# Kernel tuning notes

Measured on AMD Instinct MI355X. Metric: run time of the kernel, lower is better.

Reference implementation:

```python
import jax, jax.numpy as jnp
import numpy as np
import math

HGT, WID = 24, 24          # shape2d
NUM_HEADS = 12
EMB = 768
HEAD_DIM = EMB // NUM_HEADS
N_GRID = HGT * WID         # 576 spatial tokens
N_TOK = N_GRID + 1         # +1 CLS token
BATCH = 32


def _rel_indices(h: int, w: int) -> np.ndarray:
    """[(h*w), (h*w)] indices into the (2h-1)*(2w-1) relative table."""
    y = np.arange(h)
    x = np.arange(w)
    y1, x1, y2, x2 = np.meshgrid(y, x, y, x, indexing='ij')
    idx = (y1 - y2 + h - 1) * (2 * w - 1) + (x1 - x2 + w - 1)
    return idx.reshape(h * w, h * w)


def setup_inputs() -> dict:
    key = jax.random.key(0)
    ks = jax.random.split(key, 6)
    s = 0.02
    return {
        "x": jax.random.normal(ks[0], (BATCH, N_TOK, EMB), dtype=jnp.float32),
        "Wq": jax.random.normal(ks[1], (EMB, EMB), dtype=jnp.float32) * s,
        "bq": jnp.zeros((EMB,), dtype=jnp.float32),
        "Wk": jax.random.normal(ks[2], (EMB, EMB), dtype=jnp.float32) * s,
        "bk": jnp.zeros((EMB,), dtype=jnp.float32),
        "Wv": jax.random.normal(ks[3], (EMB, EMB), dtype=jnp.float32) * s,
        "bv": jnp.zeros((EMB,), dtype=jnp.float32),
        "Wp": jax.random.normal(ks[4], (EMB, EMB), dtype=jnp.float32) * s,
        "bp": jnp.zeros((EMB,), dtype=jnp.float32),
        "rel_table": jax.random.normal(ks[5], ((2 * HGT - 1) * (2 * WID - 1), NUM_HEADS), dtype=jnp.float32) * s,
    }


def reference(x, Wq, bq, Wk, bk, Wv, bv, Wp, bp, rel_table):
    B, N, E = x.shape
    scale = 1.0 / math.sqrt(HEAD_DIM)

    def heads(t):  # [B,N,E] -> [B,H,N,hd]
        return t.reshape(B, N, NUM_HEADS, HEAD_DIM).transpose(0, 2, 1, 3)

    q = heads(x @ Wq.T + bq)
    k = heads(x @ Wk.T + bk)
    v = heads(x @ Wv.T + bv)

    scores = jnp.einsum('bhqd,bhkd->bhqk', q, k) * scale  # [B,H,N,N]

    # relative position bias on spatial tokens (skip CLS row/col)
    idx = jnp.asarray(_rel_indices(HGT, WID))              # [Ng,Ng]
    bias = rel_table[idx].transpose(2, 0, 1)               # [H,Ng,Ng]
    scores = scores.at[:, :, 1:, 1:].add(bias)

    attn = jax.nn.softmax(scores, axis=-1)
    out = jnp.einsum('bhqk,bhkd->bhqd', attn, v)           # [B,H,N,hd]
    out = out.transpose(0, 2, 1, 3).reshape(B, N, E)
    return out @ Wp.T + bp
```

## Files before the change

### kernel.cpp

```cpp
#include <hip/hip_runtime.h>
#include <hip/hip_bf16.h>
#include <stdint.h>

#define HGT   24
#define WID   24
#define NHEAD 12
#define EMB   768
#define HD    64
#define NGRID 576
#define NTOK  577
#define NPAD  640
#define BATCH 32
#define MROWS (BATCH * NTOK)
#define NKT   10
#define NIT   5
#define NQT   5
#define QKVC  (3 * EMB)

typedef __attribute__((ext_vector_type(8))) short bf16x8;
typedef __attribute__((ext_vector_type(4))) float f32x4;

__device__ __forceinline__ short f2bf(float f) {
    union { float f; unsigned u; } c; c.f = f;
    unsigned r = (c.u + 0x7FFFu + ((c.u >> 16) & 1u)) >> 16;
    return (short)(r & 0xFFFFu);
}
__device__ __forceinline__ float b2f(short s) {
    union { unsigned u; float f; } c; c.u = ((unsigned)(unsigned short)s) << 16;
    return c.f;
}
__device__ __forceinline__ unsigned pk2bf(float a, float b) {
    __hip_bfloat162 h = __float22bfloat162_rn(make_float2(a, b));
    union { __hip_bfloat162 h; unsigned u; } c; c.h = h;
    return c.u;
}
__device__ __forceinline__ float fexp2(float x) {
#if __has_builtin(__builtin_amdgcn_exp2f)
    return __builtin_amdgcn_exp2f(x);
#else
    return __expf(x * 0.69314718f);
#endif
}

__device__ __forceinline__ void gload16(void* lds, const void* g) {
    __builtin_amdgcn_global_load_lds(
        (const __attribute__((address_space(1))) void*)g,
        (__attribute__((address_space(3))) void*)lds, 16, 0, 0);
}

__device__ __forceinline__ void wait_vm0_barrier() {
    asm volatile("s_waitcnt vmcnt(0)" ::: "memory");
    __builtin_amdgcn_s_barrier();
}

__device__ __forceinline__ int xcd_swizzle(int orig, int nwg) {
    int q = nwg >> 3, r = nwg & 7;
    int xcd = orig & 7, idx = orig >> 3;
    return (xcd < r) ? xcd * (q + 1) + idx : r * (q + 1) + (xcd - r) * q + idx;
}

__global__ void cast_f32_bf16(const float* __restrict__ src, short* __restrict__ dst, int n) {
    int i = (blockIdx.x * blockDim.x + threadIdx.x) * 4;
    int stride = gridDim.x * blockDim.x * 4;
    for (int j = i; j < n; j += stride) {
        float4 v = *(const float4*)(src + j);
        uint2 o;
        o.x = pk2bf(v.x, v.y);
        o.y = pk2bf(v.z, v.w);
        *(uint2*)(dst + j) = o;
    }
}

__global__ void bias_expand(const float* __restrict__ rel, short* __restrict__ be) {
    const float L2E = 1.44269504f;
    int q = blockIdx.x;
    int k = threadIdx.x;
    float v[NHEAD];
    if (k >= NTOK) {
#pragma unroll
        for (int h = 0; h < NHEAD; h++) v[h] = -1e30f;
    } else if (q == 0 || q >= NTOK || k == 0) {
#pragma unroll
        for (int h = 0; h < NHEAD; h++) v[h] = 0.f;
    } else {
        int i = q - 1, j = k - 1;
        int idx = ((i / WID) - (j / WID) + HGT - 1) * (2 * WID - 1)
                + ((i % WID) - (j % WID) + WID - 1);
        const float* rp = rel + (size_t)idx * NHEAD;
#pragma unroll
        for (int h = 0; h < NHEAD; h++) v[h] = rp[h];
    }
#pragma unroll
    for (int h = 0; h < NHEAD; h++)
        be[((size_t)h * NPAD + q) * NPAD + k] = f2bf(v[h] * L2E);
}

template <int MODE>
__global__ __launch_bounds__(512) void gemm_bt(
    const short* __restrict__ A, const short* __restrict__ Bw,
    const float* __restrict__ b0, const float* __restrict__ b1, const float* __restrict__ b2,
    void* __restrict__ Outp, short* __restrict__ vout, int M)
{
    constexpr int NC  = (MODE == 0) ? QKVC : EMB;
    constexpr int NBX = NC / 256;
    constexpr int K   = EMB;
    constexpr int NST = K / 32;

    __shared__ __align__(16) short Asl[4][256][32];
    __shared__ __align__(16) short Bsl[4][256][32];

    const int t    = threadIdx.x;
    const int lane = t & 63;
    const int w    = t >> 6;
    const int wm   = w >> 2;
    const int wn   = w & 3;
    const int lg   = lane >> 4;
    const int li   = lane & 15;

    const int nwg  = NBX * ((MROWS + 255) / 256);
    const int wgid = xcd_swizzle(blockIdx.x, nwg);
    const int tm   = (wgid / NBX) * 256;
    const int tn   = (wgid % NBX) * 256;

    const int drow = lane >> 2;
    const int lc   = (lane & 3) ^ ((lane >> 3) & 3);
    const int xsw  = (li >> 1) & 3;

    const short* agp[2];
    const short* bgp[2];
#pragma unroll
    for (int gi = 0; gi < 2; gi++) {
        int rm = tm + gi * 128 + w * 16 + drow; if (rm >= M) rm = M - 1;
        agp[gi] = A  + (size_t)rm * K + lc * 8;
        bgp[gi] = Bw + (size_t)(tn + gi * 128 + w * 16 + drow) * K + lc * 8;
    }

    f32x4 acc[8][4];
#pragma unroll
    for (int i = 0; i < 8; i++)
#pragma unroll
        for (int j = 0; j < 4; j++) acc[i][j] = (f32x4){0.f, 0.f, 0.f, 0.f};

#pragma unroll
    for (int ss = 0; ss < 3; ss++) {
        gload16(&Asl[ss][0 * 128 + w * 16][0], agp[0] + ss * 32);
        gload16(&Asl[ss][1 * 128 + w * 16][0], agp[1] + ss * 32);
        gload16(&Bsl[ss][0 * 128 + w * 16][0], bgp[0] + ss * 32);
        gload16(&Bsl[ss][1 * 128 + w * 16][0], bgp[1] + ss * 32);
    }

    for (int s = 0; s < NST; s++) {
        if (s < NST - 2)       asm volatile("s_waitcnt vmcnt(8)" ::: "memory");
        else if (s == NST - 2) asm volatile("s_waitcnt vmcnt(4)" ::: "memory");
        else                   asm volatile("s_waitcnt vmcnt(0)" ::: "memory");
        __builtin_amdgcn_s_barrier();

        const int cb = s & 3;
        bf16x8 af[8], bfv[4];
#pragma unroll
        for (int mi = 0; mi < 8; mi++)
            af[mi] = *(const bf16x8*)&Asl[cb][wm * 128 + mi * 16 + li][(lg ^ xsw) * 8];
#pragma unroll
        for (int nj = 0; nj < 4; nj++)
            bfv[nj] = *(const bf16x8*)&Bsl[cb][wn * 64 + nj * 16 + li][(lg ^ xsw) * 8];

        if (s + 3 < NST) {
            const int tb = (s + 3) & 3;
            const int ko = (s + 3) * 32;
            gload16(&Asl[tb][0 * 128 + w * 16][0], agp[0] + ko);
            gload16(&Asl[tb][1 * 128 + w * 16][0], agp[1] + ko);
            gload16(&Bsl[tb][0 * 128 + w * 16][0], bgp[0] + ko);
            gload16(&Bsl[tb][1 * 128 + w * 16][0], bgp[1] + ko);
        }

        __builtin_amdgcn_s_setprio(1);
#pragma unroll
        for (int mi = 0; mi < 8; mi++)
#pragma unroll
            for (int nj = 0; nj < 4; nj++)
                acc[mi][nj] = __builtin_amdgcn_mfma_f32_16x16x32_bf16(
                    bfv[nj], af[mi], acc[mi][nj], 0, 0, 0);
        __builtin_amdgcn_s_setprio(0);
    }

    if (MODE == 0 && tn >= 2 * EMB) {
#pragma unroll
        for (int nj = 0; nj < 4; nj++) {
            const int ccb = tn + wn * 64 + nj * 16 + lg * 4;
            const int e   = ccb - 2 * EMB;
            const int hh  = e >> 6, db = e & 63;
            const float4 bias4 = *(const float4*)&b2[e];
#pragma unroll
            for (int mi = 0; mi < 8; mi++) {
                int m = tm + wm * 128 + mi * 16 + li;
                if (m >= M) continue;
                int bi = m / NTOK;
                int n  = m - bi * NTOK;
                short* vr = vout + (((size_t)bi * NHEAD + hh) * HD + db) * NPAD + n;
                vr[0 * NPAD] = f2bf(acc[mi][nj][0] + bias4.x);
                vr[1 * NPAD] = f2bf(acc[mi][nj][1] + bias4.y);
                vr[2 * NPAD] = f2bf(acc[mi][nj][2] + bias4.z);
                vr[3 * NPAD] = f2bf(acc[mi][nj][3] + bias4.w);
            }
        }
    } else {
#pragma unroll
        for (int nj = 0; nj < 4; nj++) {
            const int ccb = tn + wn * 64 + nj * 16 + lg * 4;
            float4 bias4;
            if constexpr (MODE == 0) {
                int which = (ccb >= EMB) ? 1 : 0;
                const float* bb = (which == 0) ? b0 : b1;
                bias4 = *(const float4*)&bb[ccb - which * EMB];
            } else {
                bias4 = *(const float4*)&b0[ccb];
            }
#pragma unroll
            for (int mi = 0; mi < 8; mi++) {
                int m = tm + wm * 128 + mi * 16 + li;
                if (m >= M) continue;
                if constexpr (MODE == 0) {
                    uint2 o;
                    o.x = pk2bf(acc[mi][nj][0] + bias4.x, acc[mi][nj][1] + bias4.y);
                    o.y = pk2bf(acc[mi][nj][2] + bias4.z, acc[mi][nj][3] + bias4.w);
                    *(uint2*)&((short*)Outp)[(size_t)m * NC + ccb] = o;
                } else {
                    float4 o;
                    o.x = acc[mi][nj][0] + bias4.x;
                    o.y = acc[mi][nj][1] + bias4.y;
                    o.z = acc[mi][nj][2] + bias4.z;
                    o.w = acc[mi][nj][3] + bias4.w;
                    *(float4*)&((float*)Outp)[(size_t)m * NC + ccb] = o;
                }
            }
        }
    }
}

__global__ __launch_bounds__(512) void attn_kernel(
    const short* __restrict__ qnat, const short* __restrict__ vt,
    const short* __restrict__ biasx, short* __restrict__ aout)
{
    __shared__ __align__(16) short Ksl[2][2][64][64];
    __shared__ __align__(16) short Vsl[2][2][64][64];
    __shared__ __align__(16) short Psl[8][16][64];

    const int wg = (blockIdx.x & 7) * (BATCH * NHEAD * NQT / 8) + (blockIdx.x >> 3);
    const int qt = wg % NQT;
    const int rest = wg / NQT;
    const int b  = rest & 31;
    const int h  = rest >> 5;

    const int t    = threadIdx.x;
    const int lane = t & 63;
    const int w    = t >> 6;
    const int lg   = lane >> 4;
    const int li   = lane & 15;
    const int xh   = li & 7;
    const int qbase = qt * 128;
    const int myq  = qbase + w * 16 + li;

    const float SCL = 0.18033688f;

    const short* qp  = qnat + (size_t)b * NTOK * QKVC + h * HD;
    const short* kp  = qp + EMB;
    const short* vtp = vt + ((size_t)b * NHEAD + h) * (size_t)HD * NPAD;
    const short* browq = biasx + ((size_t)h * NPAD + myq) * NPAD;

    bf16x8 qf[2];
    {
        int qrow = myq < NTOK ? myq : NTOK - 1;
        qf[0] = *(const bf16x8*)(qp + (size_t)qrow * QKVC + lg * 8);
        qf[1] = *(const bf16x8*)(qp + (size_t)qrow * QKVC + 32 + lg * 8);
    }

    float mrun = -1e30f, lrun = 0.f;
    f32x4 oacc[4];
#pragma unroll
    for (int d = 0; d < 4; d++) oacc[d] = (f32x4){0.f, 0.f, 0.f, 0.f};

    const int srow = w * 8 + (lane >> 3);
    const int cofs = ((lane & 7) ^ (lane >> 3)) * 8;

#pragma unroll
    for (int st = 0; st < 2; st++) {
        int key = st * 64 + srow; if (key >= NTOK) key = NTOK - 1;
        gload16(&Ksl[0][st][w * 8][0], kp + (size_t)key * QKVC + cofs);
        gload16(&Vsl[0][st][w * 8][0], vtp + (size_t)srow * NPAD + st * 64 + cofs);
    }
    short4 bcur[2][4];
#pragma unroll
    for (int st = 0; st < 2; st++)
#pragma unroll
        for (int j = 0; j < 4; j++)
            bcur[st][j] = *(const short4*)&browq[st * 64 + j * 16 + lg * 4];
    wait_vm0_barrier();

    for (int it = 0; it < NIT; it++) {
        const int cb = it & 1, nb = cb ^ 1;

        if (it + 1 < NIT) {
#pragma unroll
            for (int st = 0; st < 2; st++) {
                int key = (it + 1) * 128 + st * 64 + srow; if (key >= NTOK) key = NTOK - 1;
                gload16(&Ksl[nb][st][w * 8][0], kp + (size_t)key * QKVC + cofs);
                gload16(&Vsl[nb][st][w * 8][0],
                        vtp + (size_t)srow * NPAD + (it + 1) * 128 + st * 64 + cofs);
            }
        }
        short4 bnxt[2][4];
        {
            int itn = (it + 1 < NIT) ? it + 1 : it;
#pragma unroll
            for (int st = 0; st < 2; st++)
#pragma unroll
                for (int j = 0; j < 4; j++)
                    bnxt[st][j] = *(const short4*)&browq[(itn * 2 + st) * 64 + j * 16 + lg * 4];
        }

        float pvv[2][4][4];
        __builtin_amdgcn_s_setprio(1);
#pragma unroll
        for (int st = 0; st < 2; st++) {
#pragma unroll
            for (int j = 0; j < 4; j++) {
                bf16x8 ak0 = *(const bf16x8*)&Ksl[cb][st][j * 16 + li][(lg ^ xh) * 8];
                bf16x8 ak1 = *(const bf16x8*)&Ksl[cb][st][j * 16 + li][((4 + lg) ^ xh) * 8];
                f32x4 s = (f32x4){0.f, 0.f, 0.f, 0.f};
                s = __builtin_amdgcn_mfma_f32_16x16x32_bf16(ak0, qf[0], s, 0, 0, 0);
                s = __builtin_amdgcn_mfma_f32_16x16x32_bf16(ak1, qf[1], s, 0, 0, 0);
                pvv[st][j][0] = fmaf(s[0], SCL, b2f(bcur[st][j].x));
                pvv[st][j][1] = fmaf(s[1], SCL, b2f(bcur[st][j].y));
                pvv[st][j][2] = fmaf(s[2], SCL, b2f(bcur[st][j].z));
                pvv[st][j][3] = fmaf(s[3], SCL, b2f(bcur[st][j].w));
            }
        }
        __builtin_amdgcn_s_setprio(0);

        float mt = pvv[0][0][0];
#pragma unroll
        for (int st = 0; st < 2; st++)
#pragma unroll
            for (int j = 0; j < 4; j++)
#pragma unroll
                for (int r = 0; r < 4; r++) mt = fmaxf(mt, pvv[st][j][r]);
        mt = fmaxf(mt, __shfl_xor(mt, 16, 64));
        mt = fmaxf(mt, __shfl_xor(mt, 32, 64));
        if (__any(mt > mrun + 8.0f)) {
            float nm  = fmaxf(mrun, mt);
            float fac = fexp2(mrun - nm);
            mrun = nm;
            lrun *= fac;
#pragma unroll
            for (int d = 0; d < 4; d++) oacc[d] *= fac;
        }
        float rs = 0.f;
#pragma unroll
        for (int st = 0; st < 2; st++)
#pragma unroll
            for (int j = 0; j < 4; j++)
#pragma unroll
                for (int r = 0; r < 4; r++) {
                    float p = fexp2(pvv[st][j][r] - mrun);
                    pvv[st][j][r] = p;
                    rs += p;
                }
        rs += __shfl_xor(rs, 16, 64);
        rs += __shfl_xor(rs, 32, 64);
        lrun += rs;

#pragma unroll
        for (int st = 0; st < 2; st++) {
#pragma unroll
            for (int j = 0; j < 4; j++) {
                uint2 pw;
                pw.x = pk2bf(pvv[st][j][0], pvv[st][j][1]);
                pw.y = pk2bf(pvv[st][j][2], pvv[st][j][3]);
                *(uint2*)&Psl[w][li][(((2 * j + (lg >> 1)) ^ xh) * 8) + (lg & 1) * 4] = pw;
            }
            __builtin_amdgcn_s_setprio(1);
#pragma unroll
            for (int dd = 0; dd < 4; dd++) {
#pragma unroll
                for (int kk = 0; kk < 2; kk++) {
                    bf16x8 av = *(const bf16x8*)&Vsl[cb][st][dd * 16 + li][((kk * 4 + lg) ^ xh) * 8];
                    bf16x8 pb = *(const bf16x8*)&Psl[w][li][((kk * 4 + lg) ^ xh) * 8];
                    oacc[dd] = __builtin_amdgcn_mfma_f32_16x16x32_bf16(av, pb, oacc[dd], 0, 0, 0);
                }
            }
            __builtin_amdgcn_s_setprio(0);
        }

        wait_vm0_barrier();
#pragma unroll
        for (int st = 0; st < 2; st++)
#pragma unroll
            for (int j = 0; j < 4; j++) bcur[st][j] = bnxt[st][j];
    }

    if (myq < NTOK) {
        float inv = 1.0f / lrun;
        short* op = aout + ((size_t)b * NTOK + myq) * EMB + h * HD;
#pragma unroll
        for (int dd = 0; dd < 4; dd++) {
            uint2 o;
            o.x = pk2bf(oacc[dd][0] * inv, oacc[dd][1] * inv);
            o.y = pk2bf(oacc[dd][2] * inv, oacc[dd][3] * inv);
            *(uint2*)&op[dd * 16 + lg * 4] = o;
        }
    }
}

extern "C" void kernel_launch(void* const* d_in, const int* in_sizes, int n_in,
                              void* d_out, int out_size, void* d_ws, size_t ws_size,
                              hipStream_t stream) {
    (void)in_sizes; (void)n_in; (void)out_size; (void)ws_size;
    const float* x   = (const float*)d_in[0];
    const float* Wq  = (const float*)d_in[1];
    const float* bq  = (const float*)d_in[2];
    const float* Wk  = (const float*)d_in[3];
    const float* bk  = (const float*)d_in[4];
    const float* Wv  = (const float*)d_in[5];
    const float* bv  = (const float*)d_in[6];
    const float* Wp  = (const float*)d_in[7];
    const float* bp  = (const float*)d_in[8];
    const float* rel = (const float*)d_in[9];

    const size_t WN = (size_t)EMB * EMB;
    short* Wb   = (short*)d_ws;
    short* Wpb  = Wb + 3 * WN;
    short* qnat = Wpb + WN;
    short* xb   = qnat + (size_t)MROWS * QKVC;
    short* aout = xb;
    short* vtb  = xb + (size_t)MROWS * EMB;
    short* bexp = vtb + (size_t)BATCH * NHEAD * HD * NPAD;

    const int XN = MROWS * EMB;
    const int MT = (MROWS + 255) / 256;
    cast_f32_bf16<<<576, 256, 0, stream>>>(Wq, Wb, (int)WN);
    cast_f32_bf16<<<576, 256, 0, stream>>>(Wk, Wb + WN, (int)WN);
    cast_f32_bf16<<<576, 256, 0, stream>>>(Wv, Wb + 2 * WN, (int)WN);
    cast_f32_bf16<<<576, 256, 0, stream>>>(Wp, Wpb, (int)WN);
    cast_f32_bf16<<<13848, 256, 0, stream>>>(x, xb, XN);
    bias_expand<<<NPAD, NPAD, 0, stream>>>(rel, bexp);

    gemm_bt<0><<<9 * MT, 512, 0, stream>>>(xb, Wb, bq, bk, bv, qnat, vtb, MROWS);
    attn_kernel<<<BATCH * NHEAD * NQT, 512, 0, stream>>>(qnat, vtb, bexp, aout);
    gemm_bt<1><<<3 * MT, 512, 0, stream>>>(aout, Wpb, bp, bp, bp, d_out, nullptr, MROWS);
}
```

Measured before the change: 265.7 us.

## Process two 16-query tiles per wave to reuse K/V LDS fragments

The attention kernel now uses 256 threads (4 waves) per block, with each wave owning 32 query rows as two 16-row sub-tiles, so each K and V fragment read from LDS feeds two MFMAs. The staging loads are split so 4 waves still fill the 128-key K/V tiles, and the bias prefetch for the next iteration moves after the PV compute. This cuts LDS read traffic per FLOP and halves the P scratch buffer. The cost is roughly double the register use per thread (two sets of accumulators, scores and Q fragments), which may lower occupancy or cause spills, and fewer waves are left to hide latency.

```diff
diff --git a/kernel.cpp b/kernel.cpp
--- a/kernel.cpp
+++ b/kernel.cpp
@@ -237,13 +237,13 @@
     }
 }
 
-__global__ __launch_bounds__(512) void attn_kernel(
+__global__ __launch_bounds__(256) void attn_kernel(
     const short* __restrict__ qnat, const short* __restrict__ vt,
     const short* __restrict__ biasx, short* __restrict__ aout)
 {
     __shared__ __align__(16) short Ksl[2][2][64][64];
     __shared__ __align__(16) short Vsl[2][2][64][64];
-    __shared__ __align__(16) short Psl[8][16][64];
+    __shared__ __align__(16) short Psl[4][16][64];
 
     const int wg = (blockIdx.x & 7) * (BATCH * NHEAD * NQT / 8) + (blockIdx.x >> 3);
     const int qt = wg % NQT;
@@ -258,42 +258,51 @@
     const int li   = lane & 15;
     const int xh   = li & 7;
     const int qbase = qt * 128;
-    const int myq  = qbase + w * 16 + li;
+    const int myq[2] = { qbase + w * 32 + li, qbase + w * 32 + 16 + li };
 
     const float SCL = 0.18033688f;
 
     const short* qp  = qnat + (size_t)b * NTOK * QKVC + h * HD;
     const short* kp  = qp + EMB;
     const short* vtp = vt + ((size_t)b * NHEAD + h) * (size_t)HD * NPAD;
-    const short* browq = biasx + ((size_t)h * NPAD + myq) * NPAD;
-
-    bf16x8 qf[2];
-    {
-        int qrow = myq < NTOK ? myq : NTOK - 1;
-        qf[0] = *(const bf16x8*)(qp + (size_t)qrow * QKVC + lg * 8);
-        qf[1] = *(const bf16x8*)(qp + (size_t)qrow * QKVC + 32 + lg * 8);
-    }
-
-    float mrun = -1e30f, lrun = 0.f;
-    f32x4 oacc[4];
-#pragma unroll
-    for (int d = 0; d < 4; d++) oacc[d] = (f32x4){0.f, 0.f, 0.f, 0.f};
+    const short* browq[2] = { biasx + ((size_t)h * NPAD + myq[0]) * NPAD,
+                              biasx + ((size_t)h * NPAD + myq[1]) * NPAD };
+
+    bf16x8 qf[2][2];
+#pragma unroll
+    for (int q2 = 0; q2 < 2; q2++) {
+        int qrow = myq[q2] < NTOK ? myq[q2] : NTOK - 1;
+        qf[q2][0] = *(const bf16x8*)(qp + (size_t)qrow * QKVC + lg * 8);
+        qf[q2][1] = *(const bf16x8*)(qp + (size_t)qrow * QKVC + 32 + lg * 8);
+    }
+
+    float mrun[2] = { -1e30f, -1e30f }, lrun[2] = { 0.f, 0.f };
+    f32x4 oacc[2][4];
+#pragma unroll
+    for (int q2 = 0; q2 < 2; q2++)
+#pragma unroll
+        for (int d = 0; d < 4; d++) oacc[q2][d] = (f32x4){0.f, 0.f, 0.f, 0.f};
 
     const int srow = w * 8 + (lane >> 3);
     const int cofs = ((lane & 7) ^ (lane >> 3)) * 8;
 
 #pragma unroll
-    for (int st = 0; st < 2; st++) {
-        int key = st * 64 + srow; if (key >= NTOK) key = NTOK - 1;
-        gload16(&Ksl[0][st][w * 8][0], kp + (size_t)key * QKVC + cofs);
-        gload16(&Vsl[0][st][w * 8][0], vtp + (size_t)srow * NPAD + st * 64 + cofs);
-    }
-    short4 bcur[2][4];
-#pragma unroll
     for (int st = 0; st < 2; st++)
 #pragma unroll
-        for (int j = 0; j < 4; j++)
-            bcur[st][j] = *(const short4*)&browq[st * 64 + j * 16 + lg * 4];
+        for (int p = 0; p < 2; p++) {
+            int key = st * 64 + p * 32 + srow; if (key >= NTOK) key = NTOK - 1;
+            gload16(&Ksl[0][st][p * 32 + w * 8][0], kp + (size_t)key * QKVC + cofs);
+            gload16(&Vsl[0][st][p * 32 + w * 8][0],
+                    vtp + (size_t)(p * 32 + srow) * NPAD + st * 64 + cofs);
+        }
+    short4 bcur[2][2][4];
+#pragma unroll
+    for (int q2 = 0; q2 < 2; q2++)
+#pragma unroll
+        for (int st = 0; st < 2; st++)
+#pragma unroll
+            for (int j = 0; j < 4; j++)
+                bcur[q2][st][j] = *(const short4*)&browq[q2][st * 64 + j * 16 + lg * 4];
     wait_vm0_barrier();
 
     for (int it = 0; it < NIT; it++) {
@@ -301,24 +310,18 @@
 
         if (it + 1 < NIT) {
 #pragma unroll
-            for (int st = 0; st < 2; st++) {
-                int key = (it + 1) * 128 + st * 64 + srow; if (key >= NTOK) key = NTOK - 1;
-                gload16(&Ksl[nb][st][w * 8][0], kp + (size_t)key * QKVC + cofs);
-                gload16(&Vsl[nb][st][w * 8][0],
-                        vtp + (size_t)srow * NPAD + (it + 1) * 128 + st * 64 + cofs);
-            }
-        }
-        short4 bnxt[2][4];
-        {
-            int itn = (it + 1 < NIT) ? it + 1 : it;
-#pragma unroll
             for (int st = 0; st < 2; st++)
 #pragma unroll
-                for (int j = 0; j < 4; j++)
-                    bnxt[st][j] = *(const short4*)&browq[(itn * 2 + st) * 64 + j * 16 + lg * 4];
-        }
-
-        float pvv[2][4][4];
+                for (int p = 0; p < 2; p++) {
+                    int key = (it + 1) * 128 + st * 64 + p * 32 + srow;
+                    if (key >= NTOK) key = NTOK - 1;
+                    gload16(&Ksl[nb][st][p * 32 + w * 8][0], kp + (size_t)key * QKVC + cofs);
+                    gload16(&Vsl[nb][st][p * 32 + w * 8][0],
+                            vtp + (size_t)(p * 32 + srow) * NPAD + (it + 1) * 128 + st * 64 + cofs);
+                }
+        }
+
+        float pvv[2][2][4][4];
         __builtin_amdgcn_s_setprio(1);
 #pragma unroll
         for (int st = 0; st < 2; st++) {
@@ -326,87 +329,130 @@
             for (int j = 0; j < 4; j++) {
                 bf16x8 ak0 = *(const bf16x8*)&Ksl[cb][st][j * 16 + li][(lg ^ xh) * 8];
                 bf16x8 ak1 = *(const bf16x8*)&Ksl[cb][st][j * 16 + li][((4 + lg) ^ xh) * 8];
-                f32x4 s = (f32x4){0.f, 0.f, 0.f, 0.f};
-                s = __builtin_amdgcn_mfma_f32_16x16x32_bf16(ak0, qf[0], s, 0, 0, 0);
-                s = __builtin_amdgcn_mfma_f32_16x16x32_bf16(ak1, qf[1], s, 0, 0, 0);
-                pvv[st][j][0] = fmaf(s[0], SCL, b2f(bcur[st][j].x));
-                pvv[st][j][1] = fmaf(s[1], SCL, b2f(bcur[st][j].y));
-                pvv[st][j][2] = fmaf(s[2], SCL, b2f(bcur[st][j].z));
-                pvv[st][j][3] = fmaf(s[3], SCL, b2f(bcur[st][j].w));
+#pragma unroll
+                for (int q2 = 0; q2 < 2; q2++) {
+                    f32x4 s = (f32x4){0.f, 0.f, 0.f, 0.f};
+                    s = __builtin_amdgcn_mfma_f32_16x16x32_bf16(ak0, qf[q2][0], s, 0, 0, 0);
+                    s = __builtin_amdgcn_mfma_f32_16x16x32_bf16(ak1, qf[q2][1], s, 0, 0, 0);
+                    pvv[st][q2][j][0] = fmaf(s[0], SCL, b2f(bcur[q2][st][j].x));
+                    pvv[st][q2][j][1] = fmaf(s[1], SCL, b2f(bcur[q2][st][j].y));
+                    pvv[st][q2][j][2] = fmaf(s[2], SCL, b2f(bcur[q2][st][j].z));
+                    pvv[st][q2][j][3] = fmaf(s[3], SCL, b2f(bcur[q2][st][j].w));
+                }
             }
         }
         __builtin_amdgcn_s_setprio(0);
 
-        float mt = pvv[0][0][0];
-#pragma unroll
-        for (int st = 0; st < 2; st++)
-#pragma unroll
-            for (int j = 0; j < 4; j++)
-#pragma unroll
-                for (int r = 0; r < 4; r++) mt = fmaxf(mt, pvv[st][j][r]);
-        mt = fmaxf(mt, __shfl_xor(mt, 16, 64));
-        mt = fmaxf(mt, __shfl_xor(mt, 32, 64));
-        if (__any(mt > mrun + 8.0f)) {
-            float nm  = fmaxf(mrun, mt);
-            float fac = fexp2(mrun - nm);
-            mrun = nm;
-            lrun *= fac;
-#pragma unroll
-            for (int d = 0; d < 4; d++) oacc[d] *= fac;
-        }
-        float rs = 0.f;
-#pragma unroll
-        for (int st = 0; st < 2; st++)
-#pragma unroll
-            for (int j = 0; j < 4; j++)
-#pragma unroll
-                for (int r = 0; r < 4; r++) {
-                    float p = fexp2(pvv[st][j][r] - mrun);
-                    pvv[st][j][r] = p;
-                    rs += p;
+        float mt[2];
+#pragma unroll
+        for (int q2 = 0; q2 < 2; q2++) {
+            float m = pvv[0][q2][0][0];
+#pragma unroll
+            for (int st = 0; st < 2; st++)
+#pragma unroll
+                for (int j = 0; j < 4; j++)
+#pragma unroll
+                    for (int r = 0; r < 4; r++) m = fmaxf(m, pvv[st][q2][j][r]);
+            m = fmaxf(m, __shfl_xor(m, 16, 64));
+            m = fmaxf(m, __shfl_xor(m, 32, 64));
+            mt[q2] = m;
+        }
+        bool need = (mt[0] > mrun[0] + 8.0f) || (mt[1] > mrun[1] + 8.0f);
+        if (__any(need)) {
+#pragma unroll
+            for (int q2 = 0; q2 < 2; q2++) {
+                float nm  = fmaxf(mrun[q2], mt[q2]);
+                float fac = fexp2(mrun[q2] - nm);
+                mrun[q2] = nm;
+                lrun[q2] *= fac;
+#pragma unroll
+                for (int d = 0; d < 4; d++) oacc[q2][d] *= fac;
+            }
+        }
+#pragma unroll
+        for (int q2 = 0; q2 < 2; q2++) {
+            float rs = 0.f;
+#pragma unroll
+            for (int st = 0; st < 2; st++)
+#pragma unroll
+                for (int j = 0; j < 4; j++)
+#pragma unroll
+                    for (int r = 0; r < 4; r++) {
+                        float p = fexp2(pvv[st][q2][j][r] - mrun[q2]);
+                        pvv[st][q2][j][r] = p;
+                        rs += p;
+                    }
+            rs += __shfl_xor(rs, 16, 64);
+            rs += __shfl_xor(rs, 32, 64);
+            lrun[q2] += rs;
+        }
+
+#pragma unroll
+        for (int st = 0; st < 2; st++) {
+            bf16x8 av[4][2];
+#pragma unroll
+            for (int dd = 0; dd < 4; dd++)
+#pragma unroll
+                for (int kk = 0; kk < 2; kk++)
+                    av[dd][kk] = *(const bf16x8*)&Vsl[cb][st][dd * 16 + li][((kk * 4 + lg) ^ xh) * 8];
+#pragma unroll
+            for (int q2 = 0; q2 < 2; q2++) {
+#pragma unroll
+                for (int j = 0; j < 4; j++) {
+                    uint2 pw;
+                    pw.x = pk2bf(pvv[st][q2][j][0], pvv[st][q2][j][1]);
+                    pw.y = pk2bf(pvv[st][q2][j][2], pvv[st][q2][j][3]);
+                    *(uint2*)&Psl[w][li][(((2 * j + (lg >> 1)) ^ xh) * 8) + (lg & 1) * 4] = pw;
                 }
-        rs += __shfl_xor(rs, 16, 64);
-        rs += __shfl_xor(rs, 32, 64);
-        lrun += rs;
-
-#pragma unroll
-        for (int st = 0; st < 2; st++) {
-#pragma unroll
-            for (int j = 0; j < 4; j++) {
-                uint2 pw;
-                pw.x = pk2bf(pvv[st][j][0], pvv[st][j][1]);
-                pw.y = pk2bf(pvv[st][j][2], pvv[st][j][3]);
-                *(uint2*)&Psl[w][li][(((2 * j + (lg >> 1)) ^ xh) * 8) + (lg & 1) * 4] = pw;
-            }
-            __builtin_amdgcn_s_setprio(1);
+                bf16x8 pb[2];
+#pragma unroll
+                for (int kk = 0; kk < 2; kk++)
+                    pb[kk] = *(const bf16x8*)&Psl[w][li][((kk * 4 + lg) ^ xh) * 8];
+                __builtin_amdgcn_s_setprio(1);
+#pragma unroll
+                for (int dd = 0; dd < 4; dd++)
+#pragma unroll
+                    for (int kk = 0; kk < 2; kk++)
+                        oacc[q2][dd] = __builtin_amdgcn_mfma_f32_16x16x32_bf16(
+                            av[dd][kk], pb[kk], oacc[q2][dd], 0, 0, 0);
+                __builtin_amdgcn_s_setprio(0);
+            }
+        }
+
+        short4 bnxt[2][2][4];
+        {
+            int itn = (it + 1 < NIT) ? it + 1 : it;
+#pragma unroll
+            for (int q2 = 0; q2 < 2; q2++)
+#pragma unroll
+                for (int st = 0; st < 2; st++)
+#pragma unroll
+                    for (int j = 0; j < 4; j++)
+                        bnxt[q2][st][j] =
+                            *(const short4*)&browq[q2][(itn * 2 + st) * 64 + j * 16 + lg * 4];
+        }
+
+        wait_vm0_barrier();
+#pragma unroll
+        for (int q2 = 0; q2 < 2; q2++)
+#pragma unroll
+            for (int st = 0; st < 2; st++)
+#pragma unroll
+                for (int j = 0; j < 4; j++) bcur[q2][st][j] = bnxt[q2][st][j];
+    }
+
+#pragma unroll
+    for (int q2 = 0; q2 < 2; q2++) {
+        if (myq[q2] < NTOK) {
+            float inv = 1.0f / lrun[q2];
+            short* op = aout + ((size_t)b * NTOK + myq[q2]) * EMB + h * HD;
 #pragma unroll
             for (int dd = 0; dd < 4; dd++) {
-#pragma unroll
-                for (int kk = 0; kk < 2; kk++) {
-                    bf16x8 av = *(const bf16x8*)&Vsl[cb][st][dd * 16 + li][((kk * 4 + lg) ^ xh) * 8];
-                    bf16x8 pb = *(const bf16x8*)&Psl[w][li][((kk * 4 + lg) ^ xh) * 8];
-                    oacc[dd] = __builtin_amdgcn_mfma_f32_16x16x32_bf16(av, pb, oacc[dd], 0, 0, 0);
-                }
-            }
-            __builtin_amdgcn_s_setprio(0);
-        }
-
-        wait_vm0_barrier();
-#pragma unroll
-        for (int st = 0; st < 2; st++)
-#pragma unroll
-            for (int j = 0; j < 4; j++) bcur[st][j] = bnxt[st][j];
-    }
-
-    if (myq < NTOK) {
-        float inv = 1.0f / lrun;
-        short* op = aout + ((size_t)b * NTOK + myq) * EMB + h * HD;
-#pragma unroll
-        for (int dd = 0; dd < 4; dd++) {
-            uint2 o;
-            o.x = pk2bf(oacc[dd][0] * inv, oacc[dd][1] * inv);
-            o.y = pk2bf(oacc[dd][2] * inv, oacc[dd][3] * inv);
-            *(uint2*)&op[dd * 16 + lg * 4] = o;
+                uint2 o;
+                o.x = pk2bf(oacc[q2][dd][0] * inv, oacc[q2][dd][1] * inv);
+                o.y = pk2bf(oacc[q2][dd][2] * inv, oacc[q2][dd][3] * inv);
+                *(uint2*)&op[dd * 16 + lg * 4] = o;
+            }
         }
     }
 }
@@ -445,6 +491,6 @@
     bias_expand<<<NPAD, NPAD, 0, stream>>>(rel, bexp);
 
     gemm_bt<0><<<9 * MT, 512, 0, stream>>>(xb, Wb, bq, bk, bv, qnat, vtb, MROWS);
-    attn_kernel<<<BATCH * NHEAD * NQT, 512, 0, stream>>>(qnat, vtb, bexp, aout);
+    attn_kernel<<<BATCH * NHEAD * NQT, 256, 0, stream>>>(qnat, vtb, bexp, aout);
     gemm_bt<1><<<3 * MT, 512, 0, stream>>>(aout, Wpb, bp, bp, bp, d_out, nullptr, MROWS);
 }
```

Result: slower. 299.6 us (+12.8%).
